# Kernel tuning notes

Hardware: AMD Instinct MI355X
Metric: run time of the kernel (lower is better)

## Reference

```python
import jax, jax.numpy as jnp
import numpy as np

N = 2_000_000
IN_CH = 10
OUT_HALF = 32  # out_channel // 2 since last_layer=False
V = 50_000


def _bn(x, gamma, beta, eps):
    # BatchNorm1d in training mode: batch stats, biased variance
    m = jnp.mean(x, axis=0)
    v = jnp.var(x, axis=0)
    return (x - m) * jax.lax.rsqrt(v + eps) * gamma + beta


def _finite_or_zero(x):
    # torch_scatter fills empty segments with 0; jax segment_min/max give +/-inf
    return jnp.where(jnp.isfinite(x), x, 0.0)


def setup_inputs() -> dict:
    key = jax.random.key(0)
    ks = jax.random.split(key, 12)
    s = lambda *sh: 0.05
    inp = {
        "inputs": jax.random.normal(ks[0], (N, IN_CH), dtype=jnp.float32),
        "unq_inv": jax.random.randint(ks[1], (N,), 0, V, dtype=jnp.int32),
        "num_segments": V,
        # self.linear: in_channel -> out_half
        "W_lin": jax.random.normal(ks[2], (IN_CH, OUT_HALF), jnp.float32) * 0.3,
        "b_lin": jnp.zeros((OUT_HALF,), jnp.float32),
        # self.norm (BN, eps=1e-3)
        "g_norm": jnp.ones((OUT_HALF,), jnp.float32),
        "be_norm": jnp.zeros((OUT_HALF,), jnp.float32),
        # self.w = Linear -> BN -> ReLU -> Linear(->1)
        "W_w1": jax.random.normal(ks[3], (IN_CH, OUT_HALF), jnp.float32) * 0.3,
        "b_w1": jnp.zeros((OUT_HALF,), jnp.float32),
        "g_wbn": jnp.ones((OUT_HALF,), jnp.float32),
        "be_wbn": jnp.zeros((OUT_HALF,), jnp.float32),
        "W_w2": jax.random.normal(ks[4], (OUT_HALF, 1), jnp.float32) * 0.3,
        "b_w2": jnp.zeros((1,), jnp.float32),
        # ChannelAttn: fc1 out_half -> 2*out_half, fc2 -> out_half
        "W_fc1": jax.random.normal(ks[5], (OUT_HALF, 2 * OUT_HALF), jnp.float32) * 0.2,
        "b_fc1": jnp.zeros((2 * OUT_HALF,), jnp.float32),
        "W_fc2": jax.random.normal(ks[6], (2 * OUT_HALF, OUT_HALF), jnp.float32) * 0.2,
        "b_fc2": jnp.zeros((OUT_HALF,), jnp.float32),
    }
    return inp


def reference(inputs, unq_inv, num_segments, W_lin, b_lin, g_norm, be_norm,
              W_w1, b_w1, g_wbn, be_wbn, W_w2, b_w2,
              W_fc1, b_fc1, W_fc2, b_fc2):
    V_ = num_segments
    v = inputs @ W_lin + b_lin                      # [N, C]
    norm_v = _bn(v, g_norm, be_norm, 1e-3)
    x = jax.nn.relu(norm_v)                         # [N, C]

    # scatter_max over pillars
    q_max = _finite_or_zero(jax.ops.segment_max(x, unq_inv, num_segments=V_))  # [V, C]

    # weight branch: Linear -> BN -> ReLU -> Linear(1), then scatter_softmax
    h = jax.nn.relu(_bn(inputs @ W_w1 + b_w1, g_wbn, be_wbn, 1e-5))
    weight = h @ W_w2 + b_w2                        # [N, 1]
    w_max = jax.ops.segment_max(weight, unq_inv, num_segments=V_)
    w_max = _finite_or_zero(w_max)
    e = jnp.exp(weight - w_max[unq_inv])            # [N, 1]
    denom = jax.ops.segment_sum(e, unq_inv, num_segments=V_)
    soft_weight = e / jnp.maximum(denom, 1e-16)[unq_inv]

    # scatter_mean(soft_weight * v)
    sw_v = soft_weight * v                          # [N, C]
    seg_sum = jax.ops.segment_sum(sw_v, unq_inv, num_segments=V_)
    cnt = jax.ops.segment_sum(jnp.ones((inputs.shape[0], 1), v.dtype), unq_inv, num_segments=V_)
    weight_x = seg_sum / jnp.maximum(cnt, 1.0)      # [V, C]

    # channel attention from scatter_min of norm_v
    min_feat = _finite_or_zero(jax.ops.segment_min(norm_v, unq_inv, num_segments=V_))
    cw = jax.nn.sigmoid(jax.nn.relu(min_feat @ W_fc1 + b_fc1) @ W_fc2 + b_fc2)  # [V, C]

    final_feat = cw * q_max + (1.0 - cw) * weight_x  # [V, C]
    return jnp.concatenate([x, final_feat[unq_inv]], axis=-1)  # [N, 2C]
```

## Files before the change

kernel.cpp:

```cpp
#include <hip/hip_runtime.h>
#include <math.h>

#define VSEG 50000
#define CH 32
#define KIN 10
#define NB_STATS 512
#define STATS_B 256
#define SCAN_B 256
#define NBLK_SCAN ((VSEG + SCAN_B - 1) / SCAN_B)
#define SEGS_PER_BLOCK 4

__global__ __launch_bounds__(256) void init_cnt_k(unsigned* cnt) {
    int i = blockIdx.x * blockDim.x + threadIdx.x;
    if (i < VSEG) cnt[i] = 0u;
}

__global__ __launch_bounds__(STATS_B) void stats_partial_k(const float* __restrict__ in,
                                                           const int* __restrict__ idx, int n,
                                                           float* __restrict__ partial,
                                                           unsigned* __restrict__ cnt,
                                                           unsigned* __restrict__ rank) {
    float acc[65];
#pragma unroll
    for (int q = 0; q < 65; ++q) acc[q] = 0.0f;

    for (int i = blockIdx.x * blockDim.x + threadIdx.x; i < n; i += gridDim.x * blockDim.x) {
        const float* ip = in + (size_t)i * KIN;
        float x[KIN];
#pragma unroll
        for (int k = 0; k < KIN; ++k) x[k] = ip[k];
#pragma unroll
        for (int k = 0; k < KIN; ++k) acc[k] += x[k];
#pragma unroll
        for (int k = 0; k < KIN; ++k) {
#pragma unroll
            for (int l = k; l < KIN; ++l)
                acc[10 + k * (21 - k) / 2 + (l - k)] += x[k] * x[l];
        }
        rank[i] = atomicAdd(&cnt[idx[i]], 1u);
    }

    __shared__ float red[STATS_B / 64][65];
    int lane = threadIdx.x & 63, wid = threadIdx.x >> 6;
#pragma unroll
    for (int q = 0; q < 65; ++q) {
        float v = acc[q];
#pragma unroll
        for (int off = 32; off > 0; off >>= 1) v += __shfl_down(v, off, 64);
        if (lane == 0) red[wid][q] = v;
    }
    __syncthreads();
    if (threadIdx.x < 65) {
        float s = 0.0f;
#pragma unroll
        for (int w = 0; w < STATS_B / 64; ++w) s += red[w][threadIdx.x];
        partial[blockIdx.x * 65 + threadIdx.x] = s;
    }
}

__global__ __launch_bounds__(128) void stats_finalize_k(
    const float* __restrict__ partial, int nb, int n,
    const float* __restrict__ Wlin, const float* __restrict__ blin,
    const float* __restrict__ g1, const float* __restrict__ be1,
    const float* __restrict__ Ww1, const float* __restrict__ bw1,
    const float* __restrict__ g2, const float* __restrict__ be2,
    float* __restrict__ ss) {
    __shared__ double tot[65];
    int t = threadIdx.x;
    if (t < 65) {
        double s = 0.0;
        for (int b = 0; b < nb; ++b) s += (double)partial[b * 65 + t];
        tot[t] = s;
    }
    __syncthreads();
    if (t < 64) {
        int c = t & 31;
        const float* W = (t < 32) ? Wlin : Ww1;
        double bb = (double)((t < 32) ? blin[c] : bw1[c]);
        double g  = (double)((t < 32) ? g1[c] : g2[c]);
        double be = (double)((t < 32) ? be1[c] : be2[c]);
        double eps = (t < 32) ? 1e-3 : 1e-5;
        double invN = 1.0 / (double)n;
        double m0 = 0.0;
        for (int k = 0; k < KIN; ++k) m0 += tot[k] * (double)W[k * CH + c];
        m0 *= invN;
        double q0 = 0.0;
        for (int k = 0; k < KIN; ++k)
            for (int l = k; l < KIN; ++l) {
                int qi = 10 + k * (21 - k) / 2 + (l - k);
                double coef = (k == l) ? 1.0 : 2.0;
                q0 += coef * tot[qi] * (double)W[k * CH + c] * (double)W[l * CH + c];
            }
        q0 *= invN;
        double var = q0 - m0 * m0;
        double mean = m0 + bb;
        double sc = g / sqrt(var + eps);
        float scale = (float)sc;
        float shift = (float)(be - mean * sc);
        if (t < 32) { ss[c] = scale; ss[32 + c] = shift; }
        else        { ss[64 + c] = scale; ss[96 + c] = shift; }
    }
}

__global__ __launch_bounds__(256) void scan1_k(const unsigned* __restrict__ cnt,
                                               unsigned* __restrict__ segstart,
                                               unsigned* __restrict__ bsum) {
    int t = threadIdx.x;
    int i = blockIdx.x * SCAN_B + t;
    unsigned v = (i < VSEG) ? cnt[i] : 0u;
    int lane = t & 63, w = t >> 6;
    unsigned incl = v;
#pragma unroll
    for (int off = 1; off < 64; off <<= 1) {
        unsigned s = __shfl_up(incl, off, 64);
        if (lane >= off) incl += s;
    }
    __shared__ unsigned wsum[4];
    if (lane == 63) wsum[w] = incl;
    __syncthreads();
    unsigned wo = 0;
#pragma unroll
    for (int k = 0; k < 4; ++k) wo += (k < w) ? wsum[k] : 0u;
    if (i < VSEG) segstart[i] = wo + incl - v;
    if (t == SCAN_B - 1) bsum[blockIdx.x] = wo + incl;
}

__global__ __launch_bounds__(256) void scan2_k(unsigned* __restrict__ bsum, int nb) {
    int t = threadIdx.x;
    unsigned v = (t < nb) ? bsum[t] : 0u;
    int lane = t & 63, w = t >> 6;
    unsigned incl = v;
#pragma unroll
    for (int off = 1; off < 64; off <<= 1) {
        unsigned s = __shfl_up(incl, off, 64);
        if (lane >= off) incl += s;
    }
    __shared__ unsigned wsum[4];
    if (lane == 63) wsum[w] = incl;
    __syncthreads();
    unsigned wo = 0;
#pragma unroll
    for (int k = 0; k < 4; ++k) wo += (k < w) ? wsum[k] : 0u;
    if (t < nb) bsum[t] = wo + incl - v;
}

__global__ __launch_bounds__(256) void scan3_k(unsigned* __restrict__ segstart,
                                               const unsigned* __restrict__ bsum) {
    int i = blockIdx.x * SCAN_B + threadIdx.x;
    if (i < VSEG) segstart[i] += bsum[blockIdx.x];
}

__global__ __launch_bounds__(256) void scatterW_k(
    const float* __restrict__ in, const int* __restrict__ idx, int n,
    const float* __restrict__ Ww1, const float* __restrict__ bw1,
    const float* __restrict__ Ww2, const float* __restrict__ bw2,
    const float* __restrict__ ss,
    const unsigned* __restrict__ segstart, const unsigned* __restrict__ rank,
    int2* __restrict__ pw) {
    __shared__ float sWw1[KIN * CH], sbw1[CH], sWw2[CH], sssU[64];
    __shared__ float sbw2;
    for (int i = threadIdx.x; i < KIN * CH; i += blockDim.x) sWw1[i] = Ww1[i];
    for (int i = threadIdx.x; i < CH; i += blockDim.x) { sbw1[i] = bw1[i]; sWw2[i] = Ww2[i]; }
    for (int i = threadIdx.x; i < 64; i += blockDim.x) sssU[i] = ss[64 + i];
    if (threadIdx.x == 0) sbw2 = bw2[0];
    __syncthreads();

    int i = blockIdx.x * blockDim.x + threadIdx.x;
    if (i >= n) return;

    const float* ip = in + (size_t)i * KIN;
    float x[KIN];
#pragma unroll
    for (int k = 0; k < KIN; ++k) x[k] = ip[k];

    float w = sbw2;
#pragma unroll 4
    for (int c = 0; c < CH; ++c) {
        float u = sbw1[c];
#pragma unroll
        for (int k = 0; k < KIN; ++k) u = fmaf(x[k], sWw1[k * CH + c], u);
        float hu = fmaxf(fmaf(u, sssU[c], sssU[32 + c]), 0.0f);
        w = fmaf(hu, sWw2[c], w);
    }

    unsigned p = segstart[idx[i]] + rank[i];
    pw[p] = make_int2(i, __float_as_int(w));
}

__global__ __launch_bounds__(256) void mega_k(
    const float* __restrict__ in, const int2* __restrict__ pw,
    const unsigned* __restrict__ segstart, const unsigned* __restrict__ cnt,
    const float* __restrict__ Wlin, const float* __restrict__ blin,
    const float* __restrict__ ss,
    const float* __restrict__ Wfc1, const float* __restrict__ bfc1,
    const float* __restrict__ Wfc2, const float* __restrict__ bfc2,
    float* __restrict__ out) {
    __shared__ float sWlin[KIN * CH], sblin[CH], sssV[64];
    __shared__ float sW1[CH * 64], sb1[64], sW2[64 * CH], sb2[CH];
    __shared__ float qmL[SEGS_PER_BLOCK][CH], mnL[SEGS_PER_BLOCK][CH];
    __shared__ float SL[SEGS_PER_BLOCK][CH], dL[SEGS_PER_BLOCK];
    __shared__ float a1L[SEGS_PER_BLOCK][64], ffL[SEGS_PER_BLOCK][CH];
    __shared__ int mS[SEGS_PER_BLOCK];

    for (int i = threadIdx.x; i < KIN * CH; i += blockDim.x) sWlin[i] = Wlin[i];
    for (int i = threadIdx.x; i < CH; i += blockDim.x) { sblin[i] = blin[i]; sb2[i] = bfc2[i]; }
    for (int i = threadIdx.x; i < 64; i += blockDim.x) { sssV[i] = ss[i]; sb1[i] = bfc1[i]; }
    for (int i = threadIdx.x; i < CH * 64; i += blockDim.x) { sW1[i] = Wfc1[i]; sW2[i] = Wfc2[i]; }
    __syncthreads();

    int lane = threadIdx.x & 63, wid = threadIdx.x >> 6;
    int c = lane & 31, h = lane >> 5;
    int seg = blockIdx.x * SEGS_PER_BLOCK + wid;

    int m = 0; unsigned base = 0;
    if (seg < VSEG) { m = (int)cnt[seg]; base = segstart[seg]; }
    if (lane == 0) mS[wid] = m;

    int mh = (m + 1) >> 1;
    int ps = h ? mh : 0;
    int pe = h ? m : mh;

    float scale = sssV[c], shift = sssV[32 + c], bl = sblin[c];
    float qm = 0.0f, mn = INFINITY, d = 0.0f, S = 0.0f;

    int p = ps;
    for (; p + 3 < pe; p += 4) {
        int2 q0 = pw[base + p], q1 = pw[base + p + 1];
        int2 q2 = pw[base + p + 2], q3 = pw[base + p + 3];
        const float* ip0 = in + (size_t)q0.x * KIN;
        const float* ip1 = in + (size_t)q1.x * KIN;
        const float* ip2 = in + (size_t)q2.x * KIN;
        const float* ip3 = in + (size_t)q3.x * KIN;
        float r0[KIN], r1[KIN], r2[KIN], r3[KIN];
#pragma unroll
        for (int k = 0; k < KIN; ++k) { r0[k] = ip0[k]; r1[k] = ip1[k]; r2[k] = ip2[k]; r3[k] = ip3[k]; }
        float v0 = bl, v1 = bl, v2 = bl, v3 = bl;
#pragma unroll
        for (int k = 0; k < KIN; ++k) {
            float wk = sWlin[k * CH + c];
            v0 = fmaf(r0[k], wk, v0);
            v1 = fmaf(r1[k], wk, v1);
            v2 = fmaf(r2[k], wk, v2);
            v3 = fmaf(r3[k], wk, v3);
        }
        float nv0 = fmaf(v0, scale, shift), nv1 = fmaf(v1, scale, shift);
        float nv2 = fmaf(v2, scale, shift), nv3 = fmaf(v3, scale, shift);
        float x0 = fmaxf(nv0, 0.0f), x1 = fmaxf(nv1, 0.0f);
        float x2 = fmaxf(nv2, 0.0f), x3 = fmaxf(nv3, 0.0f);
        out[(size_t)q0.x * 64 + c] = x0;
        out[(size_t)q1.x * 64 + c] = x1;
        out[(size_t)q2.x * 64 + c] = x2;
        out[(size_t)q3.x * 64 + c] = x3;
        float e0 = __expf(__int_as_float(q0.y)), e1 = __expf(__int_as_float(q1.y));
        float e2 = __expf(__int_as_float(q2.y)), e3 = __expf(__int_as_float(q3.y));
        qm = fmaxf(fmaxf(fmaxf(qm, x0), fmaxf(x1, x2)), x3);
        mn = fminf(fminf(fminf(mn, nv0), fminf(nv1, nv2)), nv3);
        d += (e0 + e1) + (e2 + e3);
        S = fmaf(e0, v0, S); S = fmaf(e1, v1, S);
        S = fmaf(e2, v2, S); S = fmaf(e3, v3, S);
    }
    for (; p < pe; ++p) {
        int2 q0 = pw[base + p];
        const float* ip0 = in + (size_t)q0.x * KIN;
        float v0 = bl;
#pragma unroll
        for (int k = 0; k < KIN; ++k) v0 = fmaf(ip0[k], sWlin[k * CH + c], v0);
        float nv0 = fmaf(v0, scale, shift);
        float x0 = fmaxf(nv0, 0.0f);
        out[(size_t)q0.x * 64 + c] = x0;
        float e0 = __expf(__int_as_float(q0.y));
        qm = fmaxf(qm, x0);
        mn = fminf(mn, nv0);
        d += e0;
        S = fmaf(e0, v0, S);
    }

    qm = fmaxf(qm, __shfl_xor(qm, 32));
    mn = fminf(mn, __shfl_xor(mn, 32));
    d += __shfl_xor(d, 32);
    S += __shfl_xor(S, 32);
    if (h == 0) {
        qmL[wid][c] = qm;
        mnL[wid][c] = (m > 0) ? mn : 0.0f;
        SL[wid][c]  = S;
    }
    if (lane == 0) dL[wid] = d;
    __syncthreads();

    {
        int sl = threadIdx.x >> 6, j = threadIdx.x & 63;
        float a = sb1[j];
#pragma unroll 8
        for (int cc = 0; cc < CH; ++cc) a = fmaf(mnL[sl][cc], sW1[cc * 64 + j], a);
        a1L[sl][j] = fmaxf(a, 0.0f);
    }
    __syncthreads();

    if (threadIdx.x < SEGS_PER_BLOCK * CH) {
        int sl = threadIdx.x >> 5, cc = threadIdx.x & 31;
        float z = sb2[cc];
#pragma unroll 8
        for (int j = 0; j < 64; ++j) z = fmaf(a1L[sl][j], sW2[j * CH + cc], z);
        float cw = 1.0f / (1.0f + __expf(-z));
        float dn = fmaxf(dL[sl], 1e-16f);
        float ct = fmaxf((float)mS[sl], 1.0f);
        float wx = SL[sl][cc] / (dn * ct);
        ffL[sl][cc] = cw * qmL[sl][cc] + (1.0f - cw) * wx;
    }
    __syncthreads();

    float ff = ffL[wid][c];
    for (p = ps; p < pe; ++p) {
        int pi = pw[base + p].x;
        out[(size_t)pi * 64 + 32 + c] = ff;
    }
}

extern "C" void kernel_launch(void* const* d_in, const int* in_sizes, int n_in,
                              void* d_out, int out_size, void* d_ws, size_t ws_size,
                              hipStream_t stream) {
    const float* inputs = (const float*)d_in[0];
    const int*   unq    = (const int*)d_in[1];
    const float* Wlin = (const float*)d_in[3];
    const float* blin = (const float*)d_in[4];
    const float* g1   = (const float*)d_in[5];
    const float* be1  = (const float*)d_in[6];
    const float* Ww1  = (const float*)d_in[7];
    const float* bw1  = (const float*)d_in[8];
    const float* g2   = (const float*)d_in[9];
    const float* be2  = (const float*)d_in[10];
    const float* Ww2  = (const float*)d_in[11];
    const float* bw2  = (const float*)d_in[12];
    const float* Wfc1 = (const float*)d_in[13];
    const float* bfc1 = (const float*)d_in[14];
    const float* Wfc2 = (const float*)d_in[15];
    const float* bfc2 = (const float*)d_in[16];

    const int N = in_sizes[0] / KIN;
    float* out = (float*)d_out;

    char* ws = (char*)d_ws;
    size_t off = 0;
    auto alloc = [&](size_t bytes) -> void* {
        void* p = ws + off;
        off += (bytes + 255) & ~(size_t)255;
        return p;
    };
    unsigned* cnt      = (unsigned*)alloc((size_t)VSEG * 4);
    unsigned* segstart = (unsigned*)alloc((size_t)VSEG * 4);
    unsigned* bsum     = (unsigned*)alloc((size_t)NBLK_SCAN * 4);
    float*    ssbuf    = (float*)   alloc(128 * 4);
    float*    partial  = (float*)   alloc((size_t)NB_STATS * 65 * 4);
    unsigned* rank     = (unsigned*)alloc((size_t)N * 4);
    int2*     pw       = (int2*)    alloc((size_t)N * 8);

    const int B = 256;
    int g_pt   = (N + B - 1) / B;
    int g_seg  = (VSEG + B - 1) / B;
    int g_mega = (VSEG + SEGS_PER_BLOCK - 1) / SEGS_PER_BLOCK;

    init_cnt_k<<<g_seg, B, 0, stream>>>(cnt);
    stats_partial_k<<<NB_STATS, STATS_B, 0, stream>>>(inputs, unq, N, partial, cnt, rank);
    stats_finalize_k<<<1, 128, 0, stream>>>(partial, NB_STATS, N,
                                            Wlin, blin, g1, be1, Ww1, bw1, g2, be2, ssbuf);
    scan1_k<<<NBLK_SCAN, SCAN_B, 0, stream>>>(cnt, segstart, bsum);
    scan2_k<<<1, SCAN_B, 0, stream>>>(bsum, NBLK_SCAN);
    scan3_k<<<NBLK_SCAN, SCAN_B, 0, stream>>>(segstart, bsum);
    scatterW_k<<<g_pt, B, 0, stream>>>(inputs, unq, N, Ww1, bw1, Ww2, bw2, ssbuf,
                                       segstart, rank, pw);
    mega_k<<<g_mega, B, 0, stream>>>(inputs, pw, segstart, cnt,
                                     Wlin, blin, ssbuf, Wfc1, bfc1, Wfc2, bfc2, out);
}
```

Before: 527.6 us.

## Write point features coalesced in point pass and broadcast segment features separately

The first output half is now computed and written as contiguous float4 rows in the per-point pass, which also precomputes exp of the softmax weight. Previously it was written as scattered per-channel stores from the segment-ordered kernel. The segment kernel now only reduces and writes a compact per-segment feature table, and a new gather kernel copies that table into the second output half with vectorized stores. The segment reduction loop is unrolled to 8 points. The cost is an extra kernel launch, a 6.4MB intermediate buffer, and higher register pressure from the 64 per-thread accumulators in the point pass.

```diff
diff --git a/kernel.cpp b/kernel.cpp
--- a/kernel.cpp
+++ b/kernel.cpp
@@ -150,56 +150,74 @@
     if (i < VSEG) segstart[i] += bsum[blockIdx.x];
 }
 
-__global__ __launch_bounds__(256) void scatterW_k(
+__global__ __launch_bounds__(256) void pointpass_k(
     const float* __restrict__ in, const int* __restrict__ idx, int n,
+    const float* __restrict__ Wlin, const float* __restrict__ blin,
     const float* __restrict__ Ww1, const float* __restrict__ bw1,
     const float* __restrict__ Ww2, const float* __restrict__ bw2,
     const float* __restrict__ ss,
     const unsigned* __restrict__ segstart, const unsigned* __restrict__ rank,
-    int2* __restrict__ pw) {
-    __shared__ float sWw1[KIN * CH], sbw1[CH], sWw2[CH], sssU[64];
+    float* __restrict__ out, int2* __restrict__ pw) {
+    __shared__ float sWlin[KIN * CH], sWw1[KIN * CH];
+    __shared__ float sblin[CH], sbw1[CH], sWw2[CH], sss[128];
     __shared__ float sbw2;
-    for (int i = threadIdx.x; i < KIN * CH; i += blockDim.x) sWw1[i] = Ww1[i];
-    for (int i = threadIdx.x; i < CH; i += blockDim.x) { sbw1[i] = bw1[i]; sWw2[i] = Ww2[i]; }
-    for (int i = threadIdx.x; i < 64; i += blockDim.x) sssU[i] = ss[64 + i];
+    for (int i = threadIdx.x; i < KIN * CH; i += blockDim.x) { sWlin[i] = Wlin[i]; sWw1[i] = Ww1[i]; }
+    for (int i = threadIdx.x; i < CH; i += blockDim.x) { sblin[i] = blin[i]; sbw1[i] = bw1[i]; sWw2[i] = Ww2[i]; }
+    for (int i = threadIdx.x; i < 128; i += blockDim.x) sss[i] = ss[i];
     if (threadIdx.x == 0) sbw2 = bw2[0];
     __syncthreads();
 
-    int i = blockIdx.x * blockDim.x + threadIdx.x;
-    if (i >= n) return;
-
-    const float* ip = in + (size_t)i * KIN;
+    int nidx = blockIdx.x * blockDim.x + threadIdx.x;
+    if (nidx >= n) return;
+
+    const float* ip = in + (size_t)nidx * KIN;
     float x[KIN];
 #pragma unroll
     for (int k = 0; k < KIN; ++k) x[k] = ip[k];
 
+    float v[CH], u[CH];
+#pragma unroll
+    for (int c = 0; c < CH; ++c) { v[c] = sblin[c]; u[c] = sbw1[c]; }
+#pragma unroll
+    for (int k = 0; k < KIN; ++k) {
+        float f = x[k];
+#pragma unroll
+        for (int c = 0; c < CH; ++c) {
+            v[c] = fmaf(f, sWlin[k * CH + c], v[c]);
+            u[c] = fmaf(f, sWw1[k * CH + c], u[c]);
+        }
+    }
+
     float w = sbw2;
-#pragma unroll 4
+#pragma unroll
     for (int c = 0; c < CH; ++c) {
-        float u = sbw1[c];
-#pragma unroll
-        for (int k = 0; k < KIN; ++k) u = fmaf(x[k], sWw1[k * CH + c], u);
-        float hu = fmaxf(fmaf(u, sssU[c], sssU[32 + c]), 0.0f);
+        float hu = fmaxf(fmaf(u[c], sss[64 + c], sss[96 + c]), 0.0f);
         w = fmaf(hu, sWw2[c], w);
-    }
-
-    unsigned p = segstart[idx[i]] + rank[i];
-    pw[p] = make_int2(i, __float_as_int(w));
-}
-
-__global__ __launch_bounds__(256) void mega_k(
+        v[c] = fmaxf(fmaf(v[c], sss[c], sss[32 + c]), 0.0f);
+    }
+
+    float4* op = (float4*)(out + (size_t)nidx * 64);
+#pragma unroll
+    for (int c8 = 0; c8 < 8; ++c8)
+        op[c8] = make_float4(v[4 * c8], v[4 * c8 + 1], v[4 * c8 + 2], v[4 * c8 + 3]);
+
+    unsigned p = segstart[idx[nidx]] + rank[nidx];
+    pw[p] = make_int2(nidx, __float_as_int(__expf(w)));
+}
+
+__global__ __launch_bounds__(256) void reduceMLP_k(
     const float* __restrict__ in, const int2* __restrict__ pw,
     const unsigned* __restrict__ segstart, const unsigned* __restrict__ cnt,
     const float* __restrict__ Wlin, const float* __restrict__ blin,
     const float* __restrict__ ss,
     const float* __restrict__ Wfc1, const float* __restrict__ bfc1,
     const float* __restrict__ Wfc2, const float* __restrict__ bfc2,
-    float* __restrict__ out) {
+    float* __restrict__ finalf) {
     __shared__ float sWlin[KIN * CH], sblin[CH], sssV[64];
     __shared__ float sW1[CH * 64], sb1[64], sW2[64 * CH], sb2[CH];
     __shared__ float qmL[SEGS_PER_BLOCK][CH], mnL[SEGS_PER_BLOCK][CH];
     __shared__ float SL[SEGS_PER_BLOCK][CH], dL[SEGS_PER_BLOCK];
-    __shared__ float a1L[SEGS_PER_BLOCK][64], ffL[SEGS_PER_BLOCK][CH];
+    __shared__ float a1L[SEGS_PER_BLOCK][64];
     __shared__ int mS[SEGS_PER_BLOCK];
 
     for (int i = threadIdx.x; i < KIN * CH; i += blockDim.x) sWlin[i] = Wlin[i];
@@ -224,40 +242,36 @@
     float qm = 0.0f, mn = INFINITY, d = 0.0f, S = 0.0f;
 
     int p = ps;
-    for (; p + 3 < pe; p += 4) {
-        int2 q0 = pw[base + p], q1 = pw[base + p + 1];
-        int2 q2 = pw[base + p + 2], q3 = pw[base + p + 3];
-        const float* ip0 = in + (size_t)q0.x * KIN;
-        const float* ip1 = in + (size_t)q1.x * KIN;
-        const float* ip2 = in + (size_t)q2.x * KIN;
-        const float* ip3 = in + (size_t)q3.x * KIN;
-        float r0[KIN], r1[KIN], r2[KIN], r3[KIN];
-#pragma unroll
-        for (int k = 0; k < KIN; ++k) { r0[k] = ip0[k]; r1[k] = ip1[k]; r2[k] = ip2[k]; r3[k] = ip3[k]; }
-        float v0 = bl, v1 = bl, v2 = bl, v3 = bl;
+    for (; p + 7 < pe; p += 8) {
+        int2 q[8];
+#pragma unroll
+        for (int b = 0; b < 8; ++b) q[b] = pw[base + p + b];
+        float r[8][KIN];
+#pragma unroll
+        for (int b = 0; b < 8; ++b) {
+            const float* ipb = in + (size_t)q[b].x * KIN;
+#pragma unroll
+            for (int k = 0; k < KIN; ++k) r[b][k] = ipb[k];
+        }
+        float vv[8];
+#pragma unroll
+        for (int b = 0; b < 8; ++b) vv[b] = bl;
 #pragma unroll
         for (int k = 0; k < KIN; ++k) {
             float wk = sWlin[k * CH + c];
-            v0 = fmaf(r0[k], wk, v0);
-            v1 = fmaf(r1[k], wk, v1);
-            v2 = fmaf(r2[k], wk, v2);
-            v3 = fmaf(r3[k], wk, v3);
-        }
-        float nv0 = fmaf(v0, scale, shift), nv1 = fmaf(v1, scale, shift);
-        float nv2 = fmaf(v2, scale, shift), nv3 = fmaf(v3, scale, shift);
-        float x0 = fmaxf(nv0, 0.0f), x1 = fmaxf(nv1, 0.0f);
-        float x2 = fmaxf(nv2, 0.0f), x3 = fmaxf(nv3, 0.0f);
-        out[(size_t)q0.x * 64 + c] = x0;
-        out[(size_t)q1.x * 64 + c] = x1;
-        out[(size_t)q2.x * 64 + c] = x2;
-        out[(size_t)q3.x * 64 + c] = x3;
-        float e0 = __expf(__int_as_float(q0.y)), e1 = __expf(__int_as_float(q1.y));
-        float e2 = __expf(__int_as_float(q2.y)), e3 = __expf(__int_as_float(q3.y));
-        qm = fmaxf(fmaxf(fmaxf(qm, x0), fmaxf(x1, x2)), x3);
-        mn = fminf(fminf(fminf(mn, nv0), fminf(nv1, nv2)), nv3);
-        d += (e0 + e1) + (e2 + e3);
-        S = fmaf(e0, v0, S); S = fmaf(e1, v1, S);
-        S = fmaf(e2, v2, S); S = fmaf(e3, v3, S);
+#pragma unroll
+            for (int b = 0; b < 8; ++b) vv[b] = fmaf(r[b][k], wk, vv[b]);
+        }
+#pragma unroll
+        for (int b = 0; b < 8; ++b) {
+            float nv = fmaf(vv[b], scale, shift);
+            float x  = fmaxf(nv, 0.0f);
+            float e  = __int_as_float(q[b].y);
+            qm = fmaxf(qm, x);
+            mn = fminf(mn, nv);
+            d += e;
+            S = fmaf(e, vv[b], S);
+        }
     }
     for (; p < pe; ++p) {
         int2 q0 = pw[base + p];
@@ -267,8 +281,7 @@
         for (int k = 0; k < KIN; ++k) v0 = fmaf(ip0[k], sWlin[k * CH + c], v0);
         float nv0 = fmaf(v0, scale, shift);
         float x0 = fmaxf(nv0, 0.0f);
-        out[(size_t)q0.x * 64 + c] = x0;
-        float e0 = __expf(__int_as_float(q0.y));
+        float e0 = __int_as_float(q0.y);
         qm = fmaxf(qm, x0);
         mn = fminf(mn, nv0);
         d += e0;
@@ -298,22 +311,30 @@
 
     if (threadIdx.x < SEGS_PER_BLOCK * CH) {
         int sl = threadIdx.x >> 5, cc = threadIdx.x & 31;
-        float z = sb2[cc];
+        int sg = blockIdx.x * SEGS_PER_BLOCK + sl;
+        if (sg < VSEG) {
+            float z = sb2[cc];
 #pragma unroll 8
-        for (int j = 0; j < 64; ++j) z = fmaf(a1L[sl][j], sW2[j * CH + cc], z);
-        float cw = 1.0f / (1.0f + __expf(-z));
-        float dn = fmaxf(dL[sl], 1e-16f);
-        float ct = fmaxf((float)mS[sl], 1.0f);
-        float wx = SL[sl][cc] / (dn * ct);
-        ffL[sl][cc] = cw * qmL[sl][cc] + (1.0f - cw) * wx;
-    }
-    __syncthreads();
-
-    float ff = ffL[wid][c];
-    for (p = ps; p < pe; ++p) {
-        int pi = pw[base + p].x;
-        out[(size_t)pi * 64 + 32 + c] = ff;
-    }
+            for (int j = 0; j < 64; ++j) z = fmaf(a1L[sl][j], sW2[j * CH + cc], z);
+            float cw = 1.0f / (1.0f + __expf(-z));
+            float dn = fmaxf(dL[sl], 1e-16f);
+            float ct = fmaxf((float)mS[sl], 1.0f);
+            float wx = SL[sl][cc] / (dn * ct);
+            finalf[(size_t)sg * CH + cc] = cw * qmL[sl][cc] + (1.0f - cw) * wx;
+        }
+    }
+}
+
+__global__ __launch_bounds__(256) void pass5_k(const int* __restrict__ idx, int n,
+                                               const float* __restrict__ finalf,
+                                               float* __restrict__ out) {
+    int nidx = blockIdx.x * blockDim.x + threadIdx.x;
+    if (nidx >= n) return;
+    int seg = idx[nidx];
+    const float4* fp = (const float4*)(finalf + (size_t)seg * CH);
+    float4* op = (float4*)(out + (size_t)nidx * 64 + 32);
+#pragma unroll
+    for (int i = 0; i < 8; ++i) op[i] = fp[i];
 }
 
 extern "C" void kernel_launch(void* const* d_in, const int* in_sizes, int n_in,
@@ -351,6 +372,7 @@
     unsigned* bsum     = (unsigned*)alloc((size_t)NBLK_SCAN * 4);
     float*    ssbuf    = (float*)   alloc(128 * 4);
     float*    partial  = (float*)   alloc((size_t)NB_STATS * 65 * 4);
+    float*    finalf   = (float*)   alloc((size_t)VSEG * CH * 4);
     unsigned* rank     = (unsigned*)alloc((size_t)N * 4);
     int2*     pw       = (int2*)    alloc((size_t)N * 8);
 
@@ -366,8 +388,9 @@
     scan1_k<<<NBLK_SCAN, SCAN_B, 0, stream>>>(cnt, segstart, bsum);
     scan2_k<<<1, SCAN_B, 0, stream>>>(bsum, NBLK_SCAN);
     scan3_k<<<NBLK_SCAN, SCAN_B, 0, stream>>>(segstart, bsum);
-    scatterW_k<<<g_pt, B, 0, stream>>>(inputs, unq, N, Ww1, bw1, Ww2, bw2, ssbuf,
-                                       segstart, rank, pw);
-    mega_k<<<g_mega, B, 0, stream>>>(inputs, pw, segstart, cnt,
-                                     Wlin, blin, ssbuf, Wfc1, bfc1, Wfc2, bfc2, out);
-}
+    pointpass_k<<<g_pt, B, 0, stream>>>(inputs, unq, N, Wlin, blin, Ww1, bw1, Ww2, bw2,
+                                        ssbuf, segstart, rank, out, pw);
+    reduceMLP_k<<<g_mega, B, 0, stream>>>(inputs, pw, segstart, cnt,
+                                          Wlin, blin, ssbuf, Wfc1, bfc1, Wfc2, bfc2, finalf);
+    pass5_k<<<g_pt, B, 0, stream>>>(unq, N, finalf, out);
+}
```

Result: slower. 743.3 us (+40.9%).

## Split segment reduction from output writing into a coalesced per-point final pass

Applied to the files above, without the earlier changes.

The fused per-segment kernel used to write both output halves through scattered 128-byte row fragments indexed by the original point id. It now writes only a per-segment final feature table. A new per-point kernel recomputes the linear/BN/ReLU half, gathers the segment feature and writes each 256-byte output row contiguously with float4 stores. The exp of the weight logit also moves into scatterW_k. In exchange the kernel reads inputs a second time, the linear layer is computed twice, and there is one extra launch plus a 6.4 MB intermediate.

```diff
diff --git a/kernel.cpp b/kernel.cpp
--- a/kernel.cpp
+++ b/kernel.cpp
@@ -184,22 +184,22 @@
     }
 
     unsigned p = segstart[idx[i]] + rank[i];
-    pw[p] = make_int2(i, __float_as_int(w));
-}
-
-__global__ __launch_bounds__(256) void mega_k(
+    pw[p] = make_int2(i, __float_as_int(__expf(w)));
+}
+
+__global__ __launch_bounds__(256) void reduceMLP_k(
     const float* __restrict__ in, const int2* __restrict__ pw,
     const unsigned* __restrict__ segstart, const unsigned* __restrict__ cnt,
     const float* __restrict__ Wlin, const float* __restrict__ blin,
     const float* __restrict__ ss,
     const float* __restrict__ Wfc1, const float* __restrict__ bfc1,
     const float* __restrict__ Wfc2, const float* __restrict__ bfc2,
-    float* __restrict__ out) {
+    float* __restrict__ finalf) {
     __shared__ float sWlin[KIN * CH], sblin[CH], sssV[64];
     __shared__ float sW1[CH * 64], sb1[64], sW2[64 * CH], sb2[CH];
     __shared__ float qmL[SEGS_PER_BLOCK][CH], mnL[SEGS_PER_BLOCK][CH];
     __shared__ float SL[SEGS_PER_BLOCK][CH], dL[SEGS_PER_BLOCK];
-    __shared__ float a1L[SEGS_PER_BLOCK][64], ffL[SEGS_PER_BLOCK][CH];
+    __shared__ float a1L[SEGS_PER_BLOCK][64];
     __shared__ int mS[SEGS_PER_BLOCK];
 
     for (int i = threadIdx.x; i < KIN * CH; i += blockDim.x) sWlin[i] = Wlin[i];
@@ -245,15 +245,9 @@
         }
         float nv0 = fmaf(v0, scale, shift), nv1 = fmaf(v1, scale, shift);
         float nv2 = fmaf(v2, scale, shift), nv3 = fmaf(v3, scale, shift);
-        float x0 = fmaxf(nv0, 0.0f), x1 = fmaxf(nv1, 0.0f);
-        float x2 = fmaxf(nv2, 0.0f), x3 = fmaxf(nv3, 0.0f);
-        out[(size_t)q0.x * 64 + c] = x0;
-        out[(size_t)q1.x * 64 + c] = x1;
-        out[(size_t)q2.x * 64 + c] = x2;
-        out[(size_t)q3.x * 64 + c] = x3;
-        float e0 = __expf(__int_as_float(q0.y)), e1 = __expf(__int_as_float(q1.y));
-        float e2 = __expf(__int_as_float(q2.y)), e3 = __expf(__int_as_float(q3.y));
-        qm = fmaxf(fmaxf(fmaxf(qm, x0), fmaxf(x1, x2)), x3);
+        float e0 = __int_as_float(q0.y), e1 = __int_as_float(q1.y);
+        float e2 = __int_as_float(q2.y), e3 = __int_as_float(q3.y);
+        qm = fmaxf(fmaxf(fmaxf(qm, fmaxf(nv0, 0.0f)), fmaxf(fmaxf(nv1, 0.0f), fmaxf(nv2, 0.0f))), fmaxf(nv3, 0.0f));
         mn = fminf(fminf(fminf(mn, nv0), fminf(nv1, nv2)), nv3);
         d += (e0 + e1) + (e2 + e3);
         S = fmaf(e0, v0, S); S = fmaf(e1, v1, S);
@@ -266,10 +260,8 @@
 #pragma unroll
         for (int k = 0; k < KIN; ++k) v0 = fmaf(ip0[k], sWlin[k * CH + c], v0);
         float nv0 = fmaf(v0, scale, shift);
-        float x0 = fmaxf(nv0, 0.0f);
-        out[(size_t)q0.x * 64 + c] = x0;
-        float e0 = __expf(__int_as_float(q0.y));
-        qm = fmaxf(qm, x0);
+        float e0 = __int_as_float(q0.y);
+        qm = fmaxf(qm, fmaxf(nv0, 0.0f));
         mn = fminf(mn, nv0);
         d += e0;
         S = fmaf(e0, v0, S);
@@ -298,22 +290,64 @@
 
     if (threadIdx.x < SEGS_PER_BLOCK * CH) {
         int sl = threadIdx.x >> 5, cc = threadIdx.x & 31;
-        float z = sb2[cc];
+        int sg = blockIdx.x * SEGS_PER_BLOCK + sl;
+        if (sg < VSEG) {
+            float z = sb2[cc];
 #pragma unroll 8
-        for (int j = 0; j < 64; ++j) z = fmaf(a1L[sl][j], sW2[j * CH + cc], z);
-        float cw = 1.0f / (1.0f + __expf(-z));
-        float dn = fmaxf(dL[sl], 1e-16f);
-        float ct = fmaxf((float)mS[sl], 1.0f);
-        float wx = SL[sl][cc] / (dn * ct);
-        ffL[sl][cc] = cw * qmL[sl][cc] + (1.0f - cw) * wx;
-    }
-    __syncthreads();
-
-    float ff = ffL[wid][c];
-    for (p = ps; p < pe; ++p) {
-        int pi = pw[base + p].x;
-        out[(size_t)pi * 64 + 32 + c] = ff;
-    }
+            for (int j = 0; j < 64; ++j) z = fmaf(a1L[sl][j], sW2[j * CH + cc], z);
+            float cw = 1.0f / (1.0f + __expf(-z));
+            float dn = fmaxf(dL[sl], 1e-16f);
+            float ct = fmaxf((float)mS[sl], 1.0f);
+            float wx = SL[sl][cc] / (dn * ct);
+            finalf[(size_t)sg * CH + cc] = cw * qmL[sl][cc] + (1.0f - cw) * wx;
+        }
+    }
+}
+
+__global__ __launch_bounds__(256) void finalpass_k(
+    const float* __restrict__ in, const int* __restrict__ idx, int n,
+    const float* __restrict__ Wlin, const float* __restrict__ blin,
+    const float* __restrict__ ss, const float* __restrict__ finalf,
+    float* __restrict__ out) {
+    __shared__ float sWlin[KIN * CH], sblin[CH], sssV[64];
+    for (int i = threadIdx.x; i < KIN * CH; i += blockDim.x) sWlin[i] = Wlin[i];
+    for (int i = threadIdx.x; i < CH; i += blockDim.x) sblin[i] = blin[i];
+    for (int i = threadIdx.x; i < 64; i += blockDim.x) sssV[i] = ss[i];
+    __syncthreads();
+
+    int nidx = blockIdx.x * blockDim.x + threadIdx.x;
+    if (nidx >= n) return;
+
+    const float* ip = in + (size_t)nidx * KIN;
+    float x[KIN];
+#pragma unroll
+    for (int k = 0; k < KIN; ++k) x[k] = ip[k];
+
+    float v[CH];
+#pragma unroll
+    for (int c = 0; c < CH; ++c) v[c] = sblin[c];
+#pragma unroll
+    for (int k = 0; k < KIN; ++k) {
+        float f = x[k];
+#pragma unroll
+        for (int c = 0; c < CH; ++c) v[c] = fmaf(f, sWlin[k * CH + c], v[c]);
+    }
+#pragma unroll
+    for (int c = 0; c < CH; ++c)
+        v[c] = fmaxf(fmaf(v[c], sssV[c], sssV[32 + c]), 0.0f);
+
+    int seg = idx[nidx];
+    const float4* fp = (const float4*)(finalf + (size_t)seg * CH);
+    float4 ff[8];
+#pragma unroll
+    for (int i = 0; i < 8; ++i) ff[i] = fp[i];
+
+    float4* op = (float4*)(out + (size_t)nidx * 64);
+#pragma unroll
+    for (int c8 = 0; c8 < 8; ++c8)
+        op[c8] = make_float4(v[4 * c8], v[4 * c8 + 1], v[4 * c8 + 2], v[4 * c8 + 3]);
+#pragma unroll
+    for (int i = 0; i < 8; ++i) op[8 + i] = ff[i];
 }
 
 extern "C" void kernel_launch(void* const* d_in, const int* in_sizes, int n_in,
@@ -351,13 +385,14 @@
     unsigned* bsum     = (unsigned*)alloc((size_t)NBLK_SCAN * 4);
     float*    ssbuf    = (float*)   alloc(128 * 4);
     float*    partial  = (float*)   alloc((size_t)NB_STATS * 65 * 4);
+    float*    finalf   = (float*)   alloc((size_t)VSEG * CH * 4);
     unsigned* rank     = (unsigned*)alloc((size_t)N * 4);
     int2*     pw       = (int2*)    alloc((size_t)N * 8);
 
     const int B = 256;
     int g_pt   = (N + B - 1) / B;
     int g_seg  = (VSEG + B - 1) / B;
-    int g_mega = (VSEG + SEGS_PER_BLOCK - 1) / SEGS_PER_BLOCK;
+    int g_red  = (VSEG + SEGS_PER_BLOCK - 1) / SEGS_PER_BLOCK;
 
     init_cnt_k<<<g_seg, B, 0, stream>>>(cnt);
     stats_partial_k<<<NB_STATS, STATS_B, 0, stream>>>(inputs, unq, N, partial, cnt, rank);
@@ -368,6 +403,7 @@
     scan3_k<<<NBLK_SCAN, SCAN_B, 0, stream>>>(segstart, bsum);
     scatterW_k<<<g_pt, B, 0, stream>>>(inputs, unq, N, Ww1, bw1, Ww2, bw2, ssbuf,
                                        segstart, rank, pw);
-    mega_k<<<g_mega, B, 0, stream>>>(inputs, pw, segstart, cnt,
-                                     Wlin, blin, ssbuf, Wfc1, bfc1, Wfc2, bfc2, out);
-}
+    reduceMLP_k<<<g_red, B, 0, stream>>>(inputs, pw, segstart, cnt,
+                                         Wlin, blin, ssbuf, Wfc1, bfc1, Wfc2, bfc2, finalf);
+    finalpass_k<<<g_pt, B, 0, stream>>>(inputs, unq, N, Wlin, blin, ssbuf, finalf, out);
+}
```

Measured after the change: 676.1 us. 28.2% more time.

## Write packed per-point records in segment order and emit x output coalesced

Applied to the files above, without the earlier changes.

The per-point kernel now also computes the normalized linear features and writes the first 32 output channels with contiguous float4 stores. It scatters a 64-byte record (10 inputs, exp(weight), point index) into segment-sorted order. The segment kernel then reads contiguous records instead of gathering input rows through an index, and no longer does scattered 4-byte stores for the x half. The cost is more workspace traffic (64 bytes per point written and read instead of 8), more registers in the point kernel, and the linear layer being computed twice.

```diff
diff --git a/kernel.cpp b/kernel.cpp
--- a/kernel.cpp
+++ b/kernel.cpp
@@ -150,45 +150,67 @@
     if (i < VSEG) segstart[i] += bsum[blockIdx.x];
 }
 
-__global__ __launch_bounds__(256) void scatterW_k(
+__global__ __launch_bounds__(256) void pointrec_k(
     const float* __restrict__ in, const int* __restrict__ idx, int n,
+    const float* __restrict__ Wlin, const float* __restrict__ blin,
     const float* __restrict__ Ww1, const float* __restrict__ bw1,
     const float* __restrict__ Ww2, const float* __restrict__ bw2,
     const float* __restrict__ ss,
     const unsigned* __restrict__ segstart, const unsigned* __restrict__ rank,
-    int2* __restrict__ pw) {
-    __shared__ float sWw1[KIN * CH], sbw1[CH], sWw2[CH], sssU[64];
+    float* __restrict__ out, float4* __restrict__ rec) {
+    __shared__ float sWlin[KIN * CH], sWw1[KIN * CH];
+    __shared__ float sblin[CH], sbw1[CH], sWw2[CH], sss[128];
     __shared__ float sbw2;
-    for (int i = threadIdx.x; i < KIN * CH; i += blockDim.x) sWw1[i] = Ww1[i];
-    for (int i = threadIdx.x; i < CH; i += blockDim.x) { sbw1[i] = bw1[i]; sWw2[i] = Ww2[i]; }
-    for (int i = threadIdx.x; i < 64; i += blockDim.x) sssU[i] = ss[64 + i];
+    for (int i = threadIdx.x; i < KIN * CH; i += blockDim.x) { sWlin[i] = Wlin[i]; sWw1[i] = Ww1[i]; }
+    for (int i = threadIdx.x; i < CH; i += blockDim.x) { sblin[i] = blin[i]; sbw1[i] = bw1[i]; sWw2[i] = Ww2[i]; }
+    for (int i = threadIdx.x; i < 128; i += blockDim.x) sss[i] = ss[i];
     if (threadIdx.x == 0) sbw2 = bw2[0];
     __syncthreads();
 
-    int i = blockIdx.x * blockDim.x + threadIdx.x;
-    if (i >= n) return;
-
-    const float* ip = in + (size_t)i * KIN;
+    int nidx = blockIdx.x * blockDim.x + threadIdx.x;
+    if (nidx >= n) return;
+
+    const float* ip = in + (size_t)nidx * KIN;
     float x[KIN];
 #pragma unroll
     for (int k = 0; k < KIN; ++k) x[k] = ip[k];
 
+    float v[CH];
+#pragma unroll
+    for (int c = 0; c < CH; ++c) v[c] = sblin[c];
+#pragma unroll
+    for (int k = 0; k < KIN; ++k) {
+        float f = x[k];
+#pragma unroll
+        for (int c = 0; c < CH; ++c) v[c] = fmaf(f, sWlin[k * CH + c], v[c]);
+    }
+
     float w = sbw2;
-#pragma unroll 4
+#pragma unroll
     for (int c = 0; c < CH; ++c) {
         float u = sbw1[c];
 #pragma unroll
         for (int k = 0; k < KIN; ++k) u = fmaf(x[k], sWw1[k * CH + c], u);
-        float hu = fmaxf(fmaf(u, sssU[c], sssU[32 + c]), 0.0f);
+        float hu = fmaxf(fmaf(u, sss[64 + c], sss[96 + c]), 0.0f);
         w = fmaf(hu, sWw2[c], w);
-    }
-
-    unsigned p = segstart[idx[i]] + rank[i];
-    pw[p] = make_int2(i, __float_as_int(w));
-}
-
-__global__ __launch_bounds__(256) void mega_k(
-    const float* __restrict__ in, const int2* __restrict__ pw,
+        v[c] = fmaxf(fmaf(v[c], sss[c], sss[32 + c]), 0.0f);
+    }
+
+    float4* op = (float4*)(out + (size_t)nidx * 64);
+#pragma unroll
+    for (int c8 = 0; c8 < 8; ++c8)
+        op[c8] = make_float4(v[4 * c8], v[4 * c8 + 1], v[4 * c8 + 2], v[4 * c8 + 3]);
+
+    unsigned p = segstart[idx[nidx]] + rank[nidx];
+    float4* rp = rec + (size_t)p * 4;
+    rp[0] = make_float4(x[0], x[1], x[2], x[3]);
+    rp[1] = make_float4(x[4], x[5], x[6], x[7]);
+    rp[2] = make_float4(x[8], x[9], __expf(w), __int_as_float(nidx));
+    rp[3] = make_float4(0.0f, 0.0f, 0.0f, 0.0f);
+}
+
+__global__ __launch_bounds__(256) void megarec_k(
+    const float4* __restrict__ rec,
     const unsigned* __restrict__ segstart, const unsigned* __restrict__ cnt,
     const float* __restrict__ Wlin, const float* __restrict__ blin,
     const float* __restrict__ ss,
@@ -223,56 +245,42 @@
     float scale = sssV[c], shift = sssV[32 + c], bl = sblin[c];
     float qm = 0.0f, mn = INFINITY, d = 0.0f, S = 0.0f;
 
+    const float* W = sWlin;
     int p = ps;
     for (; p + 3 < pe; p += 4) {
-        int2 q0 = pw[base + p], q1 = pw[base + p + 1];
-        int2 q2 = pw[base + p + 2], q3 = pw[base + p + 3];
-        const float* ip0 = in + (size_t)q0.x * KIN;
-        const float* ip1 = in + (size_t)q1.x * KIN;
-        const float* ip2 = in + (size_t)q2.x * KIN;
-        const float* ip3 = in + (size_t)q3.x * KIN;
-        float r0[KIN], r1[KIN], r2[KIN], r3[KIN];
-#pragma unroll
-        for (int k = 0; k < KIN; ++k) { r0[k] = ip0[k]; r1[k] = ip1[k]; r2[k] = ip2[k]; r3[k] = ip3[k]; }
+        const float4* rp = rec + ((size_t)base + p) * 4;
+        float4 a0 = rp[0],  a1 = rp[1],  a2 = rp[2];
+        float4 b0 = rp[4],  b1 = rp[5],  b2 = rp[6];
+        float4 c0 = rp[8],  c1 = rp[9],  c2 = rp[10];
+        float4 d0 = rp[12], d1 = rp[13], d2 = rp[14];
         float v0 = bl, v1 = bl, v2 = bl, v3 = bl;
-#pragma unroll
-        for (int k = 0; k < KIN; ++k) {
-            float wk = sWlin[k * CH + c];
-            v0 = fmaf(r0[k], wk, v0);
-            v1 = fmaf(r1[k], wk, v1);
-            v2 = fmaf(r2[k], wk, v2);
-            v3 = fmaf(r3[k], wk, v3);
-        }
+#define DOT(vv, r0_, r1_, r2_) \
+        vv = fmaf(r0_.x, W[0*CH+c], vv); vv = fmaf(r0_.y, W[1*CH+c], vv); \
+        vv = fmaf(r0_.z, W[2*CH+c], vv); vv = fmaf(r0_.w, W[3*CH+c], vv); \
+        vv = fmaf(r1_.x, W[4*CH+c], vv); vv = fmaf(r1_.y, W[5*CH+c], vv); \
+        vv = fmaf(r1_.z, W[6*CH+c], vv); vv = fmaf(r1_.w, W[7*CH+c], vv); \
+        vv = fmaf(r2_.x, W[8*CH+c], vv); vv = fmaf(r2_.y, W[9*CH+c], vv);
+        DOT(v0, a0, a1, a2) DOT(v1, b0, b1, b2) DOT(v2, c0, c1, c2) DOT(v3, d0, d1, d2)
         float nv0 = fmaf(v0, scale, shift), nv1 = fmaf(v1, scale, shift);
         float nv2 = fmaf(v2, scale, shift), nv3 = fmaf(v3, scale, shift);
-        float x0 = fmaxf(nv0, 0.0f), x1 = fmaxf(nv1, 0.0f);
-        float x2 = fmaxf(nv2, 0.0f), x3 = fmaxf(nv3, 0.0f);
-        out[(size_t)q0.x * 64 + c] = x0;
-        out[(size_t)q1.x * 64 + c] = x1;
-        out[(size_t)q2.x * 64 + c] = x2;
-        out[(size_t)q3.x * 64 + c] = x3;
-        float e0 = __expf(__int_as_float(q0.y)), e1 = __expf(__int_as_float(q1.y));
-        float e2 = __expf(__int_as_float(q2.y)), e3 = __expf(__int_as_float(q3.y));
-        qm = fmaxf(fmaxf(fmaxf(qm, x0), fmaxf(x1, x2)), x3);
+        qm = fmaxf(fmaxf(fmaxf(qm, fmaxf(nv0, 0.0f)),
+                         fmaxf(fmaxf(nv1, 0.0f), fmaxf(nv2, 0.0f))), fmaxf(nv3, 0.0f));
         mn = fminf(fminf(fminf(mn, nv0), fminf(nv1, nv2)), nv3);
-        d += (e0 + e1) + (e2 + e3);
-        S = fmaf(e0, v0, S); S = fmaf(e1, v1, S);
-        S = fmaf(e2, v2, S); S = fmaf(e3, v3, S);
+        d += (a2.z + b2.z) + (c2.z + d2.z);
+        S = fmaf(a2.z, v0, S); S = fmaf(b2.z, v1, S);
+        S = fmaf(c2.z, v2, S); S = fmaf(d2.z, v3, S);
     }
     for (; p < pe; ++p) {
-        int2 q0 = pw[base + p];
-        const float* ip0 = in + (size_t)q0.x * KIN;
+        const float4* rp = rec + ((size_t)base + p) * 4;
+        float4 a0 = rp[0], a1 = rp[1], a2 = rp[2];
         float v0 = bl;
-#pragma unroll
-        for (int k = 0; k < KIN; ++k) v0 = fmaf(ip0[k], sWlin[k * CH + c], v0);
+        DOT(v0, a0, a1, a2)
+#undef DOT
         float nv0 = fmaf(v0, scale, shift);
-        float x0 = fmaxf(nv0, 0.0f);
-        out[(size_t)q0.x * 64 + c] = x0;
-        float e0 = __expf(__int_as_float(q0.y));
-        qm = fmaxf(qm, x0);
+        qm = fmaxf(qm, fmaxf(nv0, 0.0f));
         mn = fminf(mn, nv0);
-        d += e0;
-        S = fmaf(e0, v0, S);
+        d += a2.z;
+        S = fmaf(a2.z, v0, S);
     }
 
     qm = fmaxf(qm, __shfl_xor(qm, 32));
@@ -311,7 +319,8 @@
 
     float ff = ffL[wid][c];
     for (p = ps; p < pe; ++p) {
-        int pi = pw[base + p].x;
+        float4 a2 = rec[((size_t)base + p) * 4 + 2];
+        int pi = __float_as_int(a2.w);
         out[(size_t)pi * 64 + 32 + c] = ff;
     }
 }
@@ -352,12 +361,12 @@
     float*    ssbuf    = (float*)   alloc(128 * 4);
     float*    partial  = (float*)   alloc((size_t)NB_STATS * 65 * 4);
     unsigned* rank     = (unsigned*)alloc((size_t)N * 4);
-    int2*     pw       = (int2*)    alloc((size_t)N * 8);
+    float4*   rec      = (float4*)  alloc((size_t)N * 64);
 
     const int B = 256;
-    int g_pt   = (N + B - 1) / B;
-    int g_seg  = (VSEG + B - 1) / B;
-    int g_mega = (VSEG + SEGS_PER_BLOCK - 1) / SEGS_PER_BLOCK;
+    int g_pt  = (N + B - 1) / B;
+    int g_seg = (VSEG + B - 1) / B;
+    int g_red = (VSEG + SEGS_PER_BLOCK - 1) / SEGS_PER_BLOCK;
 
     init_cnt_k<<<g_seg, B, 0, stream>>>(cnt);
     stats_partial_k<<<NB_STATS, STATS_B, 0, stream>>>(inputs, unq, N, partial, cnt, rank);
@@ -366,8 +375,8 @@
     scan1_k<<<NBLK_SCAN, SCAN_B, 0, stream>>>(cnt, segstart, bsum);
     scan2_k<<<1, SCAN_B, 0, stream>>>(bsum, NBLK_SCAN);
     scan3_k<<<NBLK_SCAN, SCAN_B, 0, stream>>>(segstart, bsum);
-    scatterW_k<<<g_pt, B, 0, stream>>>(inputs, unq, N, Ww1, bw1, Ww2, bw2, ssbuf,
-                                       segstart, rank, pw);
-    mega_k<<<g_mega, B, 0, stream>>>(inputs, pw, segstart, cnt,
-                                     Wlin, blin, ssbuf, Wfc1, bfc1, Wfc2, bfc2, out);
-}
+    pointrec_k<<<g_pt, B, 0, stream>>>(inputs, unq, N, Wlin, blin, Ww1, bw1, Ww2, bw2,
+                                       ssbuf, segstart, rank, out, rec);
+    megarec_k<<<g_red, B, 0, stream>>>(rec, segstart, cnt,
+                                       Wlin, blin, ssbuf, Wfc1, bfc1, Wfc2, bfc2, out);
+}
```

Result: slower. 644.9 us (+22.2%).
